# Kernel optimization log

Hardware: AMD Instinct MI355X
Metric: run time of the kernel (lower is better)

## Reference

```python
import jax, jax.numpy as jnp
import numpy as np

B, N, M, D_IN, D_OUT, H = 4, 2048, 2048, 512, 512, 8
HD = D_OUT // H
LN_EPS = 1e-5


def setup_inputs() -> dict:
    key = jax.random.key(0)
    ks = jax.random.split(key, 10)
    query = jax.random.normal(ks[0], (B, N, D_IN), dtype=jnp.float32)
    kee = jax.random.normal(ks[1], (B, M, D_IN), dtype=jnp.float32)
    val = jax.random.normal(ks[2], (B, M, D_IN), dtype=jnp.float32)
    mask = jax.random.randint(ks[3], (B, N, M), 0, 2, dtype=jnp.int32)
    # xavier_uniform with gain 1/sqrt(2): limit = gain * sqrt(6/(fan_in+fan_out))
    lim = (1.0 / np.sqrt(2.0)) * np.sqrt(6.0 / (D_IN + D_OUT))
    WQ = jax.random.uniform(ks[4], (D_OUT, D_IN), jnp.float32, -lim, lim)
    WK = jax.random.uniform(ks[5], (D_OUT, D_IN), jnp.float32, -lim, lim)
    WV = jax.random.uniform(ks[6], (D_OUT, D_IN), jnp.float32, -lim, lim)
    limO = (1.0 / np.sqrt(2.0)) * np.sqrt(6.0 / (D_OUT + D_OUT))
    WO = jax.random.uniform(ks[7], (D_OUT, D_OUT), jnp.float32, -limO, limO)
    bO = jnp.zeros((D_OUT,), jnp.float32)
    gamma = jnp.ones((D_OUT,), jnp.float32)
    beta = jnp.zeros((D_OUT,), jnp.float32)
    return {"query": query, "key": kee, "value": val, "mask": mask,
            "WQ": WQ, "WK": WK, "WV": WV, "WO": WO, "bO": bO,
            "gamma": gamma, "beta": beta}


def reference(query, key, value, mask, WQ, WK, WV, WO, bO, gamma, beta):
    scale = jnp.float32(1.0 / np.sqrt(HD))
    # project and split heads: [B, H, S, HD]
    Q = (query @ WQ.T).reshape(B, N, H, HD).transpose(0, 2, 1, 3)
    K = (key @ WK.T).reshape(B, M, H, HD).transpose(0, 2, 1, 3)
    V = (value @ WV.T).reshape(B, M, H, HD).transpose(0, 2, 1, 3)
    attn = jnp.einsum('bhnd,bhmd->bhnm', Q, K) * scale
    attn = jnp.where(mask[:, None, :, :] == 0, -jnp.inf, attn)
    attn = jax.nn.softmax(attn, axis=-1)  # dropout is identity in eval
    out = jnp.einsum('bhnm,bhmd->bhnd', attn, V)
    out = out.transpose(0, 2, 1, 3).reshape(B, N, D_OUT)
    out = out @ WO.T + bO
    x = out + query  # residual_proj is Identity (input_dim == output_dim)
    mu = jnp.mean(x, axis=-1, keepdims=True)
    var = jnp.var(x, axis=-1, keepdims=True)
    return (x - mu) * jax.lax.rsqrt(var + LN_EPS) * gamma + beta
```

## Files before the change

### kernel.cpp

```cpp
#include <hip/hip_runtime.h>
#include <stdint.h>

#define B_   4
#define N_   2048
#define M_   2048
#define DIN  512
#define DOUT 512
#define H_   8
#define HD_  64
#define ROWS (B_ * N_)

typedef __attribute__((ext_vector_type(8))) short bf16x8;
typedef __attribute__((ext_vector_type(4))) float f32x4;
typedef unsigned short u16;
typedef unsigned int   u32;

#if __has_builtin(__builtin_amdgcn_exp2f)
#define EXP2(x) __builtin_amdgcn_exp2f(x)
#else
#define EXP2(x) exp2f(x)
#endif

__device__ __forceinline__ u16 f2bf(float x) {
  union { float f; u32 u; } v; v.f = x;
  u32 r = (v.u + 0x7FFFu + ((v.u >> 16) & 1u)) >> 16;
  return (u16)r;
}

__device__ __forceinline__ void gld16(u16* lds, const u16* g) {
  __builtin_amdgcn_global_load_lds((const __attribute__((address_space(1))) u32*)g,
                                   (__attribute__((address_space(3))) u32*)lds, 16, 0, 0);
}

__global__ __launch_bounds__(256) void k_prep(
    const float* __restrict__ q, const float* __restrict__ k, const float* __restrict__ v,
    const float* __restrict__ wq_, const float* __restrict__ wk_,
    const float* __restrict__ wv_, const float* __restrict__ wo_,
    u16* __restrict__ qb, u16* __restrict__ kb, u16* __restrict__ vb,
    u16* __restrict__ wqb, u16* __restrict__ wkb, u16* __restrict__ wvb, u16* __restrict__ wob)
{
  const int id = blockIdx.x;
  const float* s; u16* d; size_t i;
  if (id < 6144) {
    const int seg = id >> 11;
    s = seg == 0 ? q : seg == 1 ? k : v;
    d = seg == 0 ? qb : seg == 1 ? kb : vb;
    i = (size_t)(id & 2047) * 2048 + threadIdx.x * 8;
  } else {
    const int wid = id - 6144;
    const int seg = wid >> 7;
    s = seg == 0 ? wq_ : seg == 1 ? wk_ : seg == 2 ? wv_ : wo_;
    d = seg == 0 ? wqb : seg == 1 ? wkb : seg == 2 ? wvb : wob;
    i = (size_t)(wid & 127) * 2048 + threadIdx.x * 8;
  }
  f32x4 x = *(const f32x4*)(s + i);
  f32x4 y = *(const f32x4*)(s + i + 4);
  bf16x8 r;
  r[0] = (short)f2bf(x[0]); r[1] = (short)f2bf(x[1]);
  r[2] = (short)f2bf(x[2]); r[3] = (short)f2bf(x[3]);
  r[4] = (short)f2bf(y[0]); r[5] = (short)f2bf(y[1]);
  r[6] = (short)f2bf(y[2]); r[7] = (short)f2bf(y[3]);
  *(bf16x8*)(d + i) = r;
}

__global__ __launch_bounds__(256) void k_gemm_qkv(
    const u16* __restrict__ Aq, const u16* __restrict__ Ak, const u16* __restrict__ Av,
    const u16* __restrict__ Wq, const u16* __restrict__ Wk, const u16* __restrict__ Wv,
    u16* __restrict__ Qo, u16* __restrict__ Ko, u16* __restrict__ Vt)
{
  __shared__ __align__(16) u16 At[128 * 64];
  __shared__ __align__(16) u16 Bt[128 * 64];
  const int z = blockIdx.z;
  const u16* A = z == 0 ? Aq : z == 1 ? Ak : Av;
  const u16* W = z == 0 ? Wq : z == 1 ? Wk : Wv;
  const int bm = blockIdx.y, bn = blockIdx.x;
  const int t = threadIdx.x, l = t & 63;
  const int w = t >> 6, wr = w >> 1, wc = w & 1;
  const int l15 = l & 15, lg = l >> 4;
  f32x4 acc[4][4] = {};
  const u16* ga = A + (size_t)(bm * 128 + (t >> 3)) * DIN + (t & 7) * 8;
  const u16* gb = W + (size_t)(bn * 128 + (t >> 3)) * DIN + (t & 7) * 8;
  u16* la = &At[t * 8];
  u16* lb = &Bt[t * 8];
  for (int kt = 0; kt < 8; ++kt) {
    const int k0 = kt * 64;
    #pragma unroll
    for (int s2 = 0; s2 < 4; ++s2) {
      gld16(la + s2 * 2048, ga + (size_t)s2 * 32 * DIN + k0);
      gld16(lb + s2 * 2048, gb + (size_t)s2 * 32 * DIN + k0);
    }
    __syncthreads();
    bf16x8 af[4][2], bfr[4][2];
    #pragma unroll
    for (int mi = 0; mi < 4; ++mi)
      #pragma unroll
      for (int c = 0; c < 2; ++c)
        af[mi][c] = *(const bf16x8*)&At[(wr * 64 + mi * 16 + l15) * 64 + c * 32 + lg * 8];
    #pragma unroll
    for (int ni = 0; ni < 4; ++ni)
      #pragma unroll
      for (int c = 0; c < 2; ++c)
        bfr[ni][c] = *(const bf16x8*)&Bt[(wc * 64 + ni * 16 + l15) * 64 + c * 32 + lg * 8];
    #pragma unroll
    for (int mi = 0; mi < 4; ++mi)
      #pragma unroll
      for (int ni = 0; ni < 4; ++ni) {
        acc[mi][ni] = __builtin_amdgcn_mfma_f32_16x16x32_bf16(af[mi][0], bfr[ni][0], acc[mi][ni], 0, 0, 0);
        acc[mi][ni] = __builtin_amdgcn_mfma_f32_16x16x32_bf16(af[mi][1], bfr[ni][1], acc[mi][ni], 0, 0, 0);
      }
    __syncthreads();
  }
  if (z < 2) {
    u16* C = z == 0 ? Qo : Ko;
    const float scl = z == 0 ? 0.18033688f : 1.0f;
    #pragma unroll
    for (int mi = 0; mi < 4; ++mi)
      #pragma unroll
      for (int ni = 0; ni < 4; ++ni) {
        const int m = bm * 128 + wr * 64 + mi * 16 + lg * 4;
        const int o = bn * 128 + wc * 64 + ni * 16 + l15;
        #pragma unroll
        for (int r = 0; r < 4; ++r)
          C[(size_t)(m + r) * DOUT + o] = f2bf(acc[mi][ni][r] * scl);
      }
  } else {
    #pragma unroll
    for (int mi = 0; mi < 4; ++mi)
      #pragma unroll
      for (int ni = 0; ni < 4; ++ni) {
        #pragma unroll
        for (int r = 0; r < 4; ++r) {
          const int m = bm * 128 + wr * 64 + mi * 16 + lg * 4 + r;
          const int o = bn * 128 + wc * 64 + ni * 16 + l15;
          const int bb = m >> 11, s = m & 2047;
          Vt[(size_t)(bb * 512 + o) * M_ + s] = f2bf(acc[mi][ni][r]);
        }
      }
  }
}

__global__ __launch_bounds__(256) void k_attn(
    const u16* __restrict__ Qp, const u16* __restrict__ Kp, const u16* __restrict__ Vt,
    const int* __restrict__ mask, u16* __restrict__ AO)
{
  __shared__ __align__(16) u16 KT[2][64 * 64];
  __shared__ __align__(16) u16 VT[2][64 * 64];
  const int qt = blockIdx.x, bh = blockIdx.y;
  const int b = bh >> 3, h = bh & 7;
  const int t = threadIdx.x, l = t & 63, w = t >> 6;
  const int l15 = l & 15, lg = l >> 4;

  const int srow = t >> 3;
  const int scol8 = t & 7;
  const int scol = (scol8 ^ (srow & 7)) * 8;
  const int kpr = (srow >> 5) * 32 + (((srow >> 4) & 1) * 4) + (((srow & 15) >> 2) * 8) + (srow & 3);
  const u16* gK = Kp + (size_t)(b * N_ + kpr) * DOUT + h * HD_ + scol;
  const u16* gV = Vt + (size_t)(b * 512 + h * HD_ + srow) * M_ + scol;

  const int qrow0 = qt * 128 + w * 32 + l15;
  const bf16x8 qf[2][2] = {
    { *(const bf16x8*)&Qp[((size_t)(b * N_) + qrow0) * DOUT + h * HD_ + lg * 8],
      *(const bf16x8*)&Qp[((size_t)(b * N_) + qrow0) * DOUT + h * HD_ + 32 + lg * 8] },
    { *(const bf16x8*)&Qp[((size_t)(b * N_) + qrow0 + 16) * DOUT + h * HD_ + lg * 8],
      *(const bf16x8*)&Qp[((size_t)(b * N_) + qrow0 + 16) * DOUT + h * HD_ + 32 + lg * 8] } };

  const int* mk[2] = { mask + ((size_t)(b * N_) + qrow0) * M_ + lg * 8,
                       mask + ((size_t)(b * N_) + qrow0 + 16) * M_ + lg * 8 };

  f32x4 o[2][4] = {};
  f32x4 lacc[2] = {};

  union U8 { u32 u[4]; bf16x8 v; };
  U8 ones;
  ones.u[0] = ones.u[1] = ones.u[2] = ones.u[3] = 0x3F803F80u;

  #define STAGE(buf_, m0_) do {                                   \
    const u16* gk_ = gK + (size_t)(m0_) * DOUT;                   \
    const u16* gv_ = gV + (m0_);                                  \
    u16* lk_ = &KT[buf_][t * 8];                                  \
    u16* lv_ = &VT[buf_][t * 8];                                  \
    gld16(lk_, gk_);                                              \
    gld16(lk_ + 2048, gk_ + (size_t)32 * DOUT);                   \
    gld16(lv_, gv_);                                              \
    gld16(lv_ + 2048, gv_ + (size_t)32 * M_);                     \
  } while (0)

  STAGE(0, 0);
  __syncthreads();

  for (int it = 0; it < 32; ++it) {
    const int buf = it & 1;
    const int m0 = it * 64;
    if (it + 1 < 32) STAGE(buf ^ 1, m0 + 64);

    const u16* Kb = KT[buf];
    const u16* Vb = VT[buf];
    const int xs = l15 & 7;

    bf16x8 ka[2][2][2];
    #pragma unroll
    for (int kb = 0; kb < 2; ++kb)
      #pragma unroll
      for (int u = 0; u < 2; ++u) {
        const int row = kb * 32 + u * 16 + l15;
        ka[kb][u][0] = *(const bf16x8*)&Kb[row * 64 + ((lg ^ xs) * 8)];
        ka[kb][u][1] = *(const bf16x8*)&Kb[row * 64 + (((4 + lg) ^ xs) * 8)];
      }

    U8 pa[2][2];
    #pragma unroll
    for (int s = 0; s < 2; ++s) {
      f32x4 sS[2][2];
      #pragma unroll
      for (int kb = 0; kb < 2; ++kb)
        #pragma unroll
        for (int u = 0; u < 2; ++u) {
          f32x4 z = {};
          z = __builtin_amdgcn_mfma_f32_16x16x32_bf16(ka[kb][u][0], qf[s][0], z, 0, 0, 0);
          z = __builtin_amdgcn_mfma_f32_16x16x32_bf16(ka[kb][u][1], qf[s][1], z, 0, 0, 0);
          sS[kb][u] = z;
        }
      #pragma unroll
      for (int kb = 0; kb < 2; ++kb) {
        const int4 ma  = *(const int4*)(mk[s] + m0 + kb * 32);
        const int4 mb2 = *(const int4*)(mk[s] + m0 + kb * 32 + 4);
        float e[8];
        #pragma unroll
        for (int u = 0; u < 2; ++u)
          #pragma unroll
          for (int r = 0; r < 4; ++r)
            e[u * 4 + r] = EXP2(sS[kb][u][r]);
        e[0] *= (float)ma.x;  e[1] *= (float)ma.y;  e[2] *= (float)ma.z;  e[3] *= (float)ma.w;
        e[4] *= (float)mb2.x; e[5] *= (float)mb2.y; e[6] *= (float)mb2.z; e[7] *= (float)mb2.w;
        #pragma unroll
        for (int j = 0; j < 4; ++j) {
          u32 rr;
          asm("v_cvt_pk_bf16_f32 %0, %1, %2" : "=v"(rr) : "v"(e[2 * j]), "v"(e[2 * j + 1]));
          pa[s][kb].u[j] = rr;
        }
      }
      lacc[s] = __builtin_amdgcn_mfma_f32_16x16x32_bf16(pa[s][0].v, ones.v, lacc[s], 0, 0, 0);
      lacc[s] = __builtin_amdgcn_mfma_f32_16x16x32_bf16(pa[s][1].v, ones.v, lacc[s], 0, 0, 0);
    }

    #pragma unroll
    for (int nd = 0; nd < 4; ++nd) {
      const int vrow = nd * 16 + l15;
      const bf16x8 vb0 = *(const bf16x8*)&Vb[vrow * 64 + ((lg ^ xs) * 8)];
      const bf16x8 vb1 = *(const bf16x8*)&Vb[vrow * 64 + (((4 + lg) ^ xs) * 8)];
      #pragma unroll
      for (int s = 0; s < 2; ++s) {
        o[s][nd] = __builtin_amdgcn_mfma_f32_16x16x32_bf16(pa[s][0].v, vb0, o[s][nd], 0, 0, 0);
        o[s][nd] = __builtin_amdgcn_mfma_f32_16x16x32_bf16(pa[s][1].v, vb1, o[s][nd], 0, 0, 0);
      }
    }
    __syncthreads();
  }

  #pragma unroll
  for (int s = 0; s < 2; ++s) {
    float rq[4];
    #pragma unroll
    for (int r = 0; r < 4; ++r) {
      const float ls = lacc[s][r];
      rq[r] = ls > 0.f ? 1.f / ls : 0.f;
    }
    #pragma unroll
    for (int nd = 0; nd < 4; ++nd)
      #pragma unroll
      for (int r = 0; r < 4; ++r) {
        const int q = qt * 128 + w * 32 + s * 16 + lg * 4 + r;
        AO[((size_t)(b * N_ + q)) * DOUT + h * HD_ + nd * 16 + l15] = f2bf(o[s][nd][r] * rq[r]);
      }
  }
  #undef STAGE
}

__global__ __launch_bounds__(256) void k_gemm_out(
    const u16* __restrict__ A, const u16* __restrict__ W,
    const float* __restrict__ bO, const float* __restrict__ query,
    float* __restrict__ X)
{
  __shared__ __align__(16) u16 At[128 * 64];
  __shared__ __align__(16) u16 Bt[128 * 64];
  const int bm = blockIdx.y, bn = blockIdx.x;
  const int t = threadIdx.x, l = t & 63;
  const int w = t >> 6, wr = w >> 1, wc = w & 1;
  const int l15 = l & 15, lg = l >> 4;
  f32x4 acc[4][4] = {};
  const u16* ga = A + (size_t)(bm * 128 + (t >> 3)) * DOUT + (t & 7) * 8;
  const u16* gb = W + (size_t)(bn * 128 + (t >> 3)) * DOUT + (t & 7) * 8;
  u16* la = &At[t * 8];
  u16* lb = &Bt[t * 8];
  for (int kt = 0; kt < 8; ++kt) {
    const int k0 = kt * 64;
    #pragma unroll
    for (int s2 = 0; s2 < 4; ++s2) {
      gld16(la + s2 * 2048, ga + (size_t)s2 * 32 * DOUT + k0);
      gld16(lb + s2 * 2048, gb + (size_t)s2 * 32 * DOUT + k0);
    }
    __syncthreads();
    bf16x8 af[4][2], bfr[4][2];
    #pragma unroll
    for (int mi = 0; mi < 4; ++mi)
      #pragma unroll
      for (int c = 0; c < 2; ++c)
        af[mi][c] = *(const bf16x8*)&At[(wr * 64 + mi * 16 + l15) * 64 + c * 32 + lg * 8];
    #pragma unroll
    for (int ni = 0; ni < 4; ++ni)
      #pragma unroll
      for (int c = 0; c < 2; ++c)
        bfr[ni][c] = *(const bf16x8*)&Bt[(wc * 64 + ni * 16 + l15) * 64 + c * 32 + lg * 8];
    #pragma unroll
    for (int mi = 0; mi < 4; ++mi)
      #pragma unroll
      for (int ni = 0; ni < 4; ++ni) {
        acc[mi][ni] = __builtin_amdgcn_mfma_f32_16x16x32_bf16(af[mi][0], bfr[ni][0], acc[mi][ni], 0, 0, 0);
        acc[mi][ni] = __builtin_amdgcn_mfma_f32_16x16x32_bf16(af[mi][1], bfr[ni][1], acc[mi][ni], 0, 0, 0);
      }
    __syncthreads();
  }
  #pragma unroll
  for (int mi = 0; mi < 4; ++mi)
    #pragma unroll
    for (int ni = 0; ni < 4; ++ni) {
      const int m = bm * 128 + wr * 64 + mi * 16 + lg * 4;
      const int o = bn * 128 + wc * 64 + ni * 16 + l15;
      const float bo = bO[o];
      #pragma unroll
      for (int r = 0; r < 4; ++r) {
        const size_t idx = (size_t)(m + r) * DOUT + o;
        X[idx] = acc[mi][ni][r] + bo + query[idx];
      }
    }
}

__global__ __launch_bounds__(256) void k_ln(
    const float* __restrict__ X, const float* __restrict__ gamma,
    const float* __restrict__ beta, float* __restrict__ out)
{
  const int w = threadIdx.x >> 6, l = threadIdx.x & 63;
  const int row = blockIdx.x * 4 + w;
  const float* x = X + (size_t)row * DOUT + l * 8;
  f32x4 a = *(const f32x4*)(x);
  f32x4 b = *(const f32x4*)(x + 4);
  float s = a[0] + a[1] + a[2] + a[3] + b[0] + b[1] + b[2] + b[3];
  float q = a[0]*a[0] + a[1]*a[1] + a[2]*a[2] + a[3]*a[3]
          + b[0]*b[0] + b[1]*b[1] + b[2]*b[2] + b[3]*b[3];
  #pragma unroll
  for (int m = 1; m < 64; m <<= 1) { s += __shfl_xor(s, m); q += __shfl_xor(q, m); }
  const float mean = s * (1.f / 512.f);
  const float var = q * (1.f / 512.f) - mean * mean;
  const float rstd = rsqrtf(var + 1e-5f);
  f32x4 g1 = *(const f32x4*)(gamma + l * 8);
  f32x4 g2 = *(const f32x4*)(gamma + l * 8 + 4);
  f32x4 e1 = *(const f32x4*)(beta + l * 8);
  f32x4 e2 = *(const f32x4*)(beta + l * 8 + 4);
  f32x4 r1, r2;
  #pragma unroll
  for (int i = 0; i < 4; ++i) {
    r1[i] = (a[i] - mean) * rstd * g1[i] + e1[i];
    r2[i] = (b[i] - mean) * rstd * g2[i] + e2[i];
  }
  float* op = out + (size_t)row * DOUT + l * 8;
  *(f32x4*)(op) = r1;
  *(f32x4*)(op + 4) = r2;
}

extern "C" void kernel_launch(void* const* d_in, const int* in_sizes, int n_in,
                              void* d_out, int out_size, void* d_ws, size_t ws_size,
                              hipStream_t stream)
{
  const float* query = (const float*)d_in[0];
  const float* key   = (const float*)d_in[1];
  const float* value = (const float*)d_in[2];
  const int*   mask  = (const int*)d_in[3];
  const float* WQ    = (const float*)d_in[4];
  const float* WK    = (const float*)d_in[5];
  const float* WV    = (const float*)d_in[6];
  const float* WO    = (const float*)d_in[7];
  const float* bO    = (const float*)d_in[8];
  const float* gamma = (const float*)d_in[9];
  const float* beta  = (const float*)d_in[10];
  float* out = (float*)d_out;

  char* ws = (char*)d_ws;
  size_t off = 0;
  auto alloc = [&](size_t bytes) -> char* {
    char* p = ws + off;
    off += (bytes + 255) & ~(size_t)255;
    return p;
  };
  u16* qb  = (u16*)alloc((size_t)ROWS * DIN * 2);
  u16* kb  = (u16*)alloc((size_t)ROWS * DIN * 2);
  u16* vb  = (u16*)alloc((size_t)ROWS * DIN * 2);
  u16* wq  = (u16*)alloc((size_t)DOUT * DIN * 2);
  u16* wk  = (u16*)alloc((size_t)DOUT * DIN * 2);
  u16* wv  = (u16*)alloc((size_t)DOUT * DIN * 2);
  u16* wo  = (u16*)alloc((size_t)DOUT * DIN * 2);
  u16* Qp  = (u16*)alloc((size_t)ROWS * DOUT * 2);
  u16* Kp  = (u16*)alloc((size_t)ROWS * DOUT * 2);
  u16* Vt  = (u16*)alloc((size_t)ROWS * DOUT * 2);
  u16* AO  = (u16*)alloc((size_t)ROWS * DOUT * 2);
  float* X = (float*)alloc((size_t)ROWS * DOUT * 4);

  k_prep     <<<6656, 256, 0, stream>>>(query, key, value, WQ, WK, WV, WO,
                                        qb, kb, vb, wq, wk, wv, wo);
  k_gemm_qkv <<<dim3(4, 64, 3), 256, 0, stream>>>(qb, kb, vb, wq, wk, wv, Qp, Kp, Vt);
  k_attn     <<<dim3(16, 32), 256, 0, stream>>>(Qp, Kp, Vt, mask, AO);
  k_gemm_out <<<dim3(4, 64), 256, 0, stream>>>(AO, wo, bO, query, X);
  k_ln       <<<2048, 256, 0, stream>>>(X, gamma, beta, out);
}
```

Baseline: 287.4 us.

## Bit-pack attention mask, transpose MFMA operands for vector stores, halve attention tile

The prep kernel gains extra blocks that compress the int32 mask into a bitmask using wave ballots, so the attention kernel reads 1 bit per element instead of 4 bytes. The GEMM and attention MFMAs swap operand order so each lane holds 4 consecutive output columns, which allows packed bf16 stores and float4 residual loads in the epilogues. The attention kernel now processes 64 query rows per block instead of 128, doubling the grid. In exchange, the mask is read once more in prep, and the smaller attention tile reloads K/V twice as often per query row.

```diff
diff --git a/kernel.cpp b/kernel.cpp
--- a/kernel.cpp
+++ b/kernel.cpp
@@ -12,6 +12,7 @@
 
 typedef __attribute__((ext_vector_type(8))) short bf16x8;
 typedef __attribute__((ext_vector_type(4))) float f32x4;
+typedef __attribute__((ext_vector_type(2))) unsigned int u32x2;
 typedef unsigned short u16;
 typedef unsigned int   u32;
 
@@ -27,6 +28,12 @@
   return (u16)r;
 }
 
+__device__ __forceinline__ u32 pkbf(float a, float b) {
+  u32 r;
+  asm("v_cvt_pk_bf16_f32 %0, %1, %2" : "=v"(r) : "v"(a), "v"(b));
+  return r;
+}
+
 __device__ __forceinline__ void gld16(u16* lds, const u16* g) {
   __builtin_amdgcn_global_load_lds((const __attribute__((address_space(1))) u32*)g,
                                    (__attribute__((address_space(3))) u32*)lds, 16, 0, 0);
@@ -36,10 +43,25 @@
     const float* __restrict__ q, const float* __restrict__ k, const float* __restrict__ v,
     const float* __restrict__ wq_, const float* __restrict__ wk_,
     const float* __restrict__ wv_, const float* __restrict__ wo_,
+    const int* __restrict__ mask,
     u16* __restrict__ qb, u16* __restrict__ kb, u16* __restrict__ vb,
-    u16* __restrict__ wqb, u16* __restrict__ wkb, u16* __restrict__ wvb, u16* __restrict__ wob)
+    u16* __restrict__ wqb, u16* __restrict__ wkb, u16* __restrict__ wvb, u16* __restrict__ wob,
+    u32* __restrict__ mbits)
 {
   const int id = blockIdx.x;
+  if (id >= 6656) {
+    const int id2 = id - 6656;
+    const int lane = threadIdx.x & 63;
+    const int gw = id2 * 4 + (threadIdx.x >> 6);
+    #pragma unroll 4
+    for (int it = 0; it < 32; ++it) {
+      long pos = ((long)(it * 8192 + gw)) * 64 + lane;
+      int mv = mask[pos];
+      unsigned long long bal = __ballot(mv != 0);
+      if ((lane & 31) == 0) mbits[pos >> 5] = (u32)(bal >> lane);
+    }
+    return;
+  }
   const float* s; u16* d; size_t i;
   if (id < 6144) {
     const int seg = id >> 11;
@@ -82,6 +104,8 @@
   const u16* gb = W + (size_t)(bn * 128 + (t >> 3)) * DIN + (t & 7) * 8;
   u16* la = &At[t * 8];
   u16* lb = &Bt[t * 8];
+  const u16* rowT = (z < 2) ? &Bt[wc * 64 * 64] : &At[wr * 64 * 64];
+  const u16* colT = (z < 2) ? &At[wr * 64 * 64] : &Bt[wc * 64 * 64];
   for (int kt = 0; kt < 8; ++kt) {
     const int k0 = kt * 64;
     #pragma unroll
@@ -90,23 +114,23 @@
       gld16(lb + s2 * 2048, gb + (size_t)s2 * 32 * DIN + k0);
     }
     __syncthreads();
-    bf16x8 af[4][2], bfr[4][2];
-    #pragma unroll
-    for (int mi = 0; mi < 4; ++mi)
+    bf16x8 rf[4][2], cf[4][2];
+    #pragma unroll
+    for (int i = 0; i < 4; ++i)
       #pragma unroll
       for (int c = 0; c < 2; ++c)
-        af[mi][c] = *(const bf16x8*)&At[(wr * 64 + mi * 16 + l15) * 64 + c * 32 + lg * 8];
-    #pragma unroll
-    for (int ni = 0; ni < 4; ++ni)
+        rf[i][c] = *(const bf16x8*)&rowT[(i * 16 + l15) * 64 + c * 32 + lg * 8];
+    #pragma unroll
+    for (int j = 0; j < 4; ++j)
       #pragma unroll
       for (int c = 0; c < 2; ++c)
-        bfr[ni][c] = *(const bf16x8*)&Bt[(wc * 64 + ni * 16 + l15) * 64 + c * 32 + lg * 8];
-    #pragma unroll
-    for (int mi = 0; mi < 4; ++mi)
-      #pragma unroll
-      for (int ni = 0; ni < 4; ++ni) {
-        acc[mi][ni] = __builtin_amdgcn_mfma_f32_16x16x32_bf16(af[mi][0], bfr[ni][0], acc[mi][ni], 0, 0, 0);
-        acc[mi][ni] = __builtin_amdgcn_mfma_f32_16x16x32_bf16(af[mi][1], bfr[ni][1], acc[mi][ni], 0, 0, 0);
+        cf[j][c] = *(const bf16x8*)&colT[(j * 16 + l15) * 64 + c * 32 + lg * 8];
+    #pragma unroll
+    for (int i = 0; i < 4; ++i)
+      #pragma unroll
+      for (int j = 0; j < 4; ++j) {
+        acc[i][j] = __builtin_amdgcn_mfma_f32_16x16x32_bf16(rf[i][0], cf[j][0], acc[i][j], 0, 0, 0);
+        acc[i][j] = __builtin_amdgcn_mfma_f32_16x16x32_bf16(rf[i][1], cf[j][1], acc[i][j], 0, 0, 0);
       }
     __syncthreads();
   }
@@ -114,34 +138,37 @@
     u16* C = z == 0 ? Qo : Ko;
     const float scl = z == 0 ? 0.18033688f : 1.0f;
     #pragma unroll
-    for (int mi = 0; mi < 4; ++mi)
-      #pragma unroll
-      for (int ni = 0; ni < 4; ++ni) {
-        const int m = bm * 128 + wr * 64 + mi * 16 + lg * 4;
-        const int o = bn * 128 + wc * 64 + ni * 16 + l15;
-        #pragma unroll
-        for (int r = 0; r < 4; ++r)
-          C[(size_t)(m + r) * DOUT + o] = f2bf(acc[mi][ni][r] * scl);
+    for (int i = 0; i < 4; ++i) {
+      const int o0 = bn * 128 + wc * 64 + i * 16 + lg * 4;
+      #pragma unroll
+      for (int j = 0; j < 4; ++j) {
+        const int m = bm * 128 + wr * 64 + j * 16 + l15;
+        u32x2 pr;
+        pr[0] = pkbf(acc[i][j][0] * scl, acc[i][j][1] * scl);
+        pr[1] = pkbf(acc[i][j][2] * scl, acc[i][j][3] * scl);
+        *(u32x2*)&C[(size_t)m * DOUT + o0] = pr;
       }
+    }
   } else {
     #pragma unroll
-    for (int mi = 0; mi < 4; ++mi)
-      #pragma unroll
-      for (int ni = 0; ni < 4; ++ni) {
-        #pragma unroll
-        for (int r = 0; r < 4; ++r) {
-          const int m = bm * 128 + wr * 64 + mi * 16 + lg * 4 + r;
-          const int o = bn * 128 + wc * 64 + ni * 16 + l15;
-          const int bb = m >> 11, s = m & 2047;
-          Vt[(size_t)(bb * 512 + o) * M_ + s] = f2bf(acc[mi][ni][r]);
-        }
+    for (int i = 0; i < 4; ++i) {
+      const int mm = bm * 128 + wr * 64 + i * 16 + lg * 4;
+      const int bb = mm >> 11, s = mm & 2047;
+      #pragma unroll
+      for (int j = 0; j < 4; ++j) {
+        const int o = bn * 128 + wc * 64 + j * 16 + l15;
+        u32x2 pr;
+        pr[0] = pkbf(acc[i][j][0], acc[i][j][1]);
+        pr[1] = pkbf(acc[i][j][2], acc[i][j][3]);
+        *(u32x2*)&Vt[(size_t)(bb * 512 + o) * M_ + s] = pr;
       }
+    }
   }
 }
 
 __global__ __launch_bounds__(256) void k_attn(
     const u16* __restrict__ Qp, const u16* __restrict__ Kp, const u16* __restrict__ Vt,
-    const int* __restrict__ mask, u16* __restrict__ AO)
+    const u32* __restrict__ mbits, u16* __restrict__ AO)
 {
   __shared__ __align__(16) u16 KT[2][64 * 64];
   __shared__ __align__(16) u16 VT[2][64 * 64];
@@ -157,19 +184,13 @@
   const u16* gK = Kp + (size_t)(b * N_ + kpr) * DOUT + h * HD_ + scol;
   const u16* gV = Vt + (size_t)(b * 512 + h * HD_ + srow) * M_ + scol;
 
-  const int qrow0 = qt * 128 + w * 32 + l15;
-  const bf16x8 qf[2][2] = {
-    { *(const bf16x8*)&Qp[((size_t)(b * N_) + qrow0) * DOUT + h * HD_ + lg * 8],
-      *(const bf16x8*)&Qp[((size_t)(b * N_) + qrow0) * DOUT + h * HD_ + 32 + lg * 8] },
-    { *(const bf16x8*)&Qp[((size_t)(b * N_) + qrow0 + 16) * DOUT + h * HD_ + lg * 8],
-      *(const bf16x8*)&Qp[((size_t)(b * N_) + qrow0 + 16) * DOUT + h * HD_ + 32 + lg * 8] } };
-
-  const int* mk[2] = { mask + ((size_t)(b * N_) + qrow0) * M_ + lg * 8,
-                       mask + ((size_t)(b * N_) + qrow0 + 16) * M_ + lg * 8 };
-
-  f32x4 o[2][4] = {};
-  f32x4 lacc[2] = {};
-
+  const int qrow = qt * 64 + w * 16 + l15;
+  const bf16x8 qf0 = *(const bf16x8*)&Qp[((size_t)(b * N_) + qrow) * DOUT + h * HD_ + lg * 8];
+  const bf16x8 qf1 = *(const bf16x8*)&Qp[((size_t)(b * N_) + qrow) * DOUT + h * HD_ + 32 + lg * 8];
+  const u32* mrow = mbits + ((size_t)(b * N_) + qrow) * (M_ / 32);
+
+  f32x4 o[4] = {};
+  f32x4 lacc = {};
   union U8 { u32 u[4]; bf16x8 v; };
   U8 ones;
   ones.u[0] = ones.u[1] = ones.u[2] = ones.u[3] = 0x3F803F80u;
@@ -193,85 +214,65 @@
     const int m0 = it * 64;
     if (it + 1 < 32) STAGE(buf ^ 1, m0 + 64);
 
+    const u32 mw0 = mrow[m0 >> 5];
+    const u32 mw1 = mrow[(m0 >> 5) + 1];
+
     const u16* Kb = KT[buf];
     const u16* Vb = VT[buf];
     const int xs = l15 & 7;
 
-    bf16x8 ka[2][2][2];
-    #pragma unroll
-    for (int kb = 0; kb < 2; ++kb)
+    U8 pa[2];
+    #pragma unroll
+    for (int kbk = 0; kbk < 2; ++kbk) {
+      f32x4 sS[2];
       #pragma unroll
       for (int u = 0; u < 2; ++u) {
-        const int row = kb * 32 + u * 16 + l15;
-        ka[kb][u][0] = *(const bf16x8*)&Kb[row * 64 + ((lg ^ xs) * 8)];
-        ka[kb][u][1] = *(const bf16x8*)&Kb[row * 64 + (((4 + lg) ^ xs) * 8)];
+        const int row = kbk * 32 + u * 16 + l15;
+        const bf16x8 a0 = *(const bf16x8*)&Kb[row * 64 + ((lg ^ xs) * 8)];
+        const bf16x8 a1 = *(const bf16x8*)&Kb[row * 64 + (((4 + lg) ^ xs) * 8)];
+        f32x4 zz = {};
+        zz = __builtin_amdgcn_mfma_f32_16x16x32_bf16(a0, qf0, zz, 0, 0, 0);
+        zz = __builtin_amdgcn_mfma_f32_16x16x32_bf16(a1, qf1, zz, 0, 0, 0);
+        sS[u] = zz;
       }
-
-    U8 pa[2][2];
-    #pragma unroll
-    for (int s = 0; s < 2; ++s) {
-      f32x4 sS[2][2];
-      #pragma unroll
-      for (int kb = 0; kb < 2; ++kb)
+      const u32 mw = kbk ? mw1 : mw0;
+      float e[8];
+      #pragma unroll
+      for (int u = 0; u < 2; ++u)
         #pragma unroll
-        for (int u = 0; u < 2; ++u) {
-          f32x4 z = {};
-          z = __builtin_amdgcn_mfma_f32_16x16x32_bf16(ka[kb][u][0], qf[s][0], z, 0, 0, 0);
-          z = __builtin_amdgcn_mfma_f32_16x16x32_bf16(ka[kb][u][1], qf[s][1], z, 0, 0, 0);
-          sS[kb][u] = z;
+        for (int r = 0; r < 4; ++r) {
+          const int bit = lg * 8 + u * 4 + r;
+          float p = EXP2(sS[u][r]);
+          e[u * 4 + r] = ((mw >> bit) & 1u) ? p : 0.f;
         }
-      #pragma unroll
-      for (int kb = 0; kb < 2; ++kb) {
-        const int4 ma  = *(const int4*)(mk[s] + m0 + kb * 32);
-        const int4 mb2 = *(const int4*)(mk[s] + m0 + kb * 32 + 4);
-        float e[8];
-        #pragma unroll
-        for (int u = 0; u < 2; ++u)
-          #pragma unroll
-          for (int r = 0; r < 4; ++r)
-            e[u * 4 + r] = EXP2(sS[kb][u][r]);
-        e[0] *= (float)ma.x;  e[1] *= (float)ma.y;  e[2] *= (float)ma.z;  e[3] *= (float)ma.w;
-        e[4] *= (float)mb2.x; e[5] *= (float)mb2.y; e[6] *= (float)mb2.z; e[7] *= (float)mb2.w;
-        #pragma unroll
-        for (int j = 0; j < 4; ++j) {
-          u32 rr;
-          asm("v_cvt_pk_bf16_f32 %0, %1, %2" : "=v"(rr) : "v"(e[2 * j]), "v"(e[2 * j + 1]));
-          pa[s][kb].u[j] = rr;
-        }
-      }
-      lacc[s] = __builtin_amdgcn_mfma_f32_16x16x32_bf16(pa[s][0].v, ones.v, lacc[s], 0, 0, 0);
-      lacc[s] = __builtin_amdgcn_mfma_f32_16x16x32_bf16(pa[s][1].v, ones.v, lacc[s], 0, 0, 0);
-    }
+      pa[kbk].u[0] = pkbf(e[0], e[1]);
+      pa[kbk].u[1] = pkbf(e[2], e[3]);
+      pa[kbk].u[2] = pkbf(e[4], e[5]);
+      pa[kbk].u[3] = pkbf(e[6], e[7]);
+    }
+    lacc = __builtin_amdgcn_mfma_f32_16x16x32_bf16(ones.v, pa[0].v, lacc, 0, 0, 0);
+    lacc = __builtin_amdgcn_mfma_f32_16x16x32_bf16(ones.v, pa[1].v, lacc, 0, 0, 0);
 
     #pragma unroll
     for (int nd = 0; nd < 4; ++nd) {
       const int vrow = nd * 16 + l15;
       const bf16x8 vb0 = *(const bf16x8*)&Vb[vrow * 64 + ((lg ^ xs) * 8)];
       const bf16x8 vb1 = *(const bf16x8*)&Vb[vrow * 64 + (((4 + lg) ^ xs) * 8)];
-      #pragma unroll
-      for (int s = 0; s < 2; ++s) {
-        o[s][nd] = __builtin_amdgcn_mfma_f32_16x16x32_bf16(pa[s][0].v, vb0, o[s][nd], 0, 0, 0);
-        o[s][nd] = __builtin_amdgcn_mfma_f32_16x16x32_bf16(pa[s][1].v, vb1, o[s][nd], 0, 0, 0);
-      }
+      o[nd] = __builtin_amdgcn_mfma_f32_16x16x32_bf16(vb0, pa[0].v, o[nd], 0, 0, 0);
+      o[nd] = __builtin_amdgcn_mfma_f32_16x16x32_bf16(vb1, pa[1].v, o[nd], 0, 0, 0);
     }
     __syncthreads();
   }
 
+  const float ls = lacc[0];
+  const float rq = ls > 0.f ? 1.f / ls : 0.f;
+  const size_t obase = ((size_t)(b * N_) + qrow) * DOUT + h * HD_;
   #pragma unroll
-  for (int s = 0; s < 2; ++s) {
-    float rq[4];
-    #pragma unroll
-    for (int r = 0; r < 4; ++r) {
-      const float ls = lacc[s][r];
-      rq[r] = ls > 0.f ? 1.f / ls : 0.f;
-    }
-    #pragma unroll
-    for (int nd = 0; nd < 4; ++nd)
-      #pragma unroll
-      for (int r = 0; r < 4; ++r) {
-        const int q = qt * 128 + w * 32 + s * 16 + lg * 4 + r;
-        AO[((size_t)(b * N_ + q)) * DOUT + h * HD_ + nd * 16 + l15] = f2bf(o[s][nd][r] * rq[r]);
-      }
+  for (int nd = 0; nd < 4; ++nd) {
+    u32x2 pr;
+    pr[0] = pkbf(o[nd][0] * rq, o[nd][1] * rq);
+    pr[1] = pkbf(o[nd][2] * rq, o[nd][3] * rq);
+    *(u32x2*)&AO[obase + nd * 16 + lg * 4] = pr;
   }
   #undef STAGE
 }
@@ -292,6 +293,8 @@
   const u16* gb = W + (size_t)(bn * 128 + (t >> 3)) * DOUT + (t & 7) * 8;
   u16* la = &At[t * 8];
   u16* lb = &Bt[t * 8];
+  const u16* rowT = &Bt[wc * 64 * 64];
+  const u16* colT = &At[wr * 64 * 64];
   for (int kt = 0; kt < 8; ++kt) {
     const int k0 = kt * 64;
     #pragma unroll
@@ -300,39 +303,41 @@
       gld16(lb + s2 * 2048, gb + (size_t)s2 * 32 * DOUT + k0);
     }
     __syncthreads();
-    bf16x8 af[4][2], bfr[4][2];
-    #pragma unroll
-    for (int mi = 0; mi < 4; ++mi)
+    bf16x8 rf[4][2], cf[4][2];
+    #pragma unroll
+    for (int i = 0; i < 4; ++i)
       #pragma unroll
       for (int c = 0; c < 2; ++c)
-        af[mi][c] = *(const bf16x8*)&At[(wr * 64 + mi * 16 + l15) * 64 + c * 32 + lg * 8];
-    #pragma unroll
-    for (int ni = 0; ni < 4; ++ni)
+        rf[i][c] = *(const bf16x8*)&rowT[(i * 16 + l15) * 64 + c * 32 + lg * 8];
+    #pragma unroll
+    for (int j = 0; j < 4; ++j)
       #pragma unroll
       for (int c = 0; c < 2; ++c)
-        bfr[ni][c] = *(const bf16x8*)&Bt[(wc * 64 + ni * 16 + l15) * 64 + c * 32 + lg * 8];
-    #pragma unroll
-    for (int mi = 0; mi < 4; ++mi)
-      #pragma unroll
-      for (int ni = 0; ni < 4; ++ni) {
-        acc[mi][ni] = __builtin_amdgcn_mfma_f32_16x16x32_bf16(af[mi][0], bfr[ni][0], acc[mi][ni], 0, 0, 0);
-        acc[mi][ni] = __builtin_amdgcn_mfma_f32_16x16x32_bf16(af[mi][1], bfr[ni][1], acc[mi][ni], 0, 0, 0);
+        cf[j][c] = *(const bf16x8*)&colT[(j * 16 + l15) * 64 + c * 32 + lg * 8];
+    #pragma unroll
+    for (int i = 0; i < 4; ++i)
+      #pragma unroll
+      for (int j = 0; j < 4; ++j) {
+        acc[i][j] = __builtin_amdgcn_mfma_f32_16x16x32_bf16(rf[i][0], cf[j][0], acc[i][j], 0, 0, 0);
+        acc[i][j] = __builtin_amdgcn_mfma_f32_16x16x32_bf16(rf[i][1], cf[j][1], acc[i][j], 0, 0, 0);
       }
     __syncthreads();
   }
   #pragma unroll
-  for (int mi = 0; mi < 4; ++mi)
-    #pragma unroll
-    for (int ni = 0; ni < 4; ++ni) {
-      const int m = bm * 128 + wr * 64 + mi * 16 + lg * 4;
-      const int o = bn * 128 + wc * 64 + ni * 16 + l15;
-      const float bo = bO[o];
-      #pragma unroll
-      for (int r = 0; r < 4; ++r) {
-        const size_t idx = (size_t)(m + r) * DOUT + o;
-        X[idx] = acc[mi][ni][r] + bo + query[idx];
-      }
-    }
+  for (int i = 0; i < 4; ++i) {
+    const int o0 = bn * 128 + wc * 64 + i * 16 + lg * 4;
+    const f32x4 bo4 = *(const f32x4*)&bO[o0];
+    #pragma unroll
+    for (int j = 0; j < 4; ++j) {
+      const int m = bm * 128 + wr * 64 + j * 16 + l15;
+      const size_t idx = (size_t)m * DOUT + o0;
+      const f32x4 qv = *(const f32x4*)&query[idx];
+      f32x4 res;
+      #pragma unroll
+      for (int r = 0; r < 4; ++r) res[r] = acc[i][j][r] + bo4[r] + qv[r];
+      *(f32x4*)&X[idx] = res;
+    }
+  }
 }
 
 __global__ __launch_bounds__(256) void k_ln(
@@ -401,13 +406,14 @@
   u16* Qp  = (u16*)alloc((size_t)ROWS * DOUT * 2);
   u16* Kp  = (u16*)alloc((size_t)ROWS * DOUT * 2);
   u16* Vt  = (u16*)alloc((size_t)ROWS * DOUT * 2);
+  u32* mb  = (u32*)alloc((size_t)B_ * N_ * (M_ / 32) * 4);
   u16* AO  = (u16*)alloc((size_t)ROWS * DOUT * 2);
   float* X = (float*)alloc((size_t)ROWS * DOUT * 4);
 
-  k_prep     <<<6656, 256, 0, stream>>>(query, key, value, WQ, WK, WV, WO,
-                                        qb, kb, vb, wq, wk, wv, wo);
+  k_prep     <<<8704, 256, 0, stream>>>(query, key, value, WQ, WK, WV, WO, mask,
+                                        qb, kb, vb, wq, wk, wv, wo, mb);
   k_gemm_qkv <<<dim3(4, 64, 3), 256, 0, stream>>>(qb, kb, vb, wq, wk, wv, Qp, Kp, Vt);
-  k_attn     <<<dim3(16, 32), 256, 0, stream>>>(Qp, Kp, Vt, mask, AO);
+  k_attn     <<<dim3(32, 32), 256, 0, stream>>>(Qp, Kp, Vt, mb, AO);
   k_gemm_out <<<dim3(4, 64), 256, 0, stream>>>(AO, wo, bO, query, X);
   k_ln       <<<2048, 256, 0, stream>>>(X, gamma, beta, out);
 }
```

Result: faster. 274.7 us (-4.4%).
